# Optimization experiments

Hardware: AMD Instinct MI355X
Metric: run time of the kernel (lower is better)

The kernel has to match this reference:

```python
import jax, jax.numpy as jnp
import numpy as np

DIM = 1024
QK = 64
V = 64
H = 8
PD = 21
HD = QK // H  # 8
SCALE = HD ** -0.5


def _ln(x, g, b, eps=1e-5):
    mu = jnp.mean(x, axis=-1, keepdims=True)
    var = jnp.var(x, axis=-1, keepdims=True)
    return (x - mu) * jax.lax.rsqrt(var + eps) * g + b


def setup_inputs() -> dict:
    key = jax.random.key(0)
    ks = jax.random.split(key, 16)
    B, L = 2, 1024
    inp = {
        'x': jax.random.normal(ks[0], (B, L, DIM), jnp.float32),
        'pair': jax.random.normal(ks[1], (B, L, L, PD), jnp.float32),
        'mask': jnp.ones((B, L), dtype=bool),
        # attention params
        'ln_g': jnp.ones((DIM,), jnp.float32),
        'ln_b': jnp.zeros((DIM,), jnp.float32),
        'Wq': jax.random.normal(ks[2], (DIM, QK), jnp.float32) * DIM ** -0.5,
        'Wv': jax.random.normal(ks[3], (DIM, QK), jnp.float32) * DIM ** -0.5,
        'bv': jnp.zeros((QK,), jnp.float32),
        'Wg': jax.random.normal(ks[4], (DIM, V), jnp.float32) * DIM ** -0.5,
        'bg': jnp.zeros((V,), jnp.float32),
        'Wo': jax.random.normal(ks[5], (V, V), jnp.float32) * V ** -0.5,
        'bo': jnp.zeros((V,), jnp.float32),
        # pair bias params
        'pln_g': jnp.ones((PD,), jnp.float32),
        'pln_b': jnp.zeros((PD,), jnp.float32),
        'Wpb': jax.random.normal(ks[6], (PD, H), jnp.float32) * PD ** -0.5,
        # OuterProductMean params
        'oln_g': jnp.ones((V,), jnp.float32),
        'oln_b': jnp.zeros((V,), jnp.float32),
        'Wr': jax.random.normal(ks[7], (V, 16), jnp.float32) * V ** -0.5,
        'br': jnp.zeros((16,), jnp.float32),
        'Wout': jax.random.normal(ks[8], (256, PD), jnp.float32) * 256 ** -0.5,
        'bout': jnp.zeros((PD,), jnp.float32),
    }
    return inp


def reference(x, pair, mask, ln_g, ln_b, Wq, Wv, bv, Wg, bg, Wo, bo,
              pln_g, pln_b, Wpb, oln_g, oln_b, Wr, br, Wout, bout):
    B, L, _ = x.shape
    nx = _ln(x, ln_g, ln_b)
    # NB: original code computes k with to_q as well (k = self.to_q(normed_x))
    q = (nx @ Wq).reshape(B, L, H, HD).transpose(0, 2, 1, 3)  # b h l d
    k = (nx @ Wq).reshape(B, L, H, HD).transpose(0, 2, 1, 3)
    v = (nx @ Wv + bv).reshape(B, L, H, HD).transpose(0, 2, 1, 3)
    gate = jax.nn.sigmoid(nx @ Wg + bg)  # b l v
    sim = jnp.einsum('bhid,bhjd->bhij', q, k) * SCALE
    bias = _ln(pair, pln_g, pln_b) @ Wpb  # b i j h
    sim = sim + jnp.transpose(bias, (0, 3, 1, 2))
    sim = jnp.where(mask[:, None, None, :], sim, -jnp.inf)
    attn = jax.nn.softmax(sim, axis=-1)
    out = jnp.einsum('bhij,bhjd->bhid', attn, v)
    out = out.transpose(0, 2, 1, 3).reshape(B, L, QK)  # b l (h d)
    out = (out * gate) @ Wo + bo  # b l v
    # OuterProductMean: out_pair[b,m,n,p] = sum_ij r[b,m,i] r[b,n,j] W3[i,j,p] + bout
    r = _ln(out, oln_g, oln_b) @ Wr + br  # b l 16
    W3 = Wout.reshape(16, 16, PD)  # flatten order (i j)
    t = jnp.einsum('bmi,ijp->bmjp', r, W3)  # b l 16 p (small)
    pair_out = jnp.einsum('bmjp,bnj->bmnp', t, r) + bout  # b m n p
    return out, pair_out
```

## Files before the change

kernel.cpp:

```cpp
#include <hip/hip_runtime.h>
#include <hip/hip_bf16.h>
#include <stdint.h>
#include <stddef.h>

typedef unsigned short u16;
typedef unsigned int   u32;

#define SCALE 0.35355339059327373f

using bfrag  = __attribute__((ext_vector_type(8))) short;
using f32x4v = __attribute__((ext_vector_type(4))) float;

__device__ __forceinline__ float bfh(u16 u) {
    union { u32 i; float f; } v; v.i = ((u32)u) << 16; return v.f;
}
__device__ __forceinline__ u16 f2bf(float f) {
    u32 x = __float_as_uint(f);
    u32 r = x + 0x7FFFu + ((x >> 16) & 1u);
    return (u16)(r >> 16);
}
__device__ __forceinline__ float dot4f(float4 a, float4 b) {
    return fmaf(a.x, b.x, fmaf(a.y, b.y, fmaf(a.z, b.z, a.w * b.w)));
}
__device__ __forceinline__ f32x4v mfma16(uint4 a, uint4 b, f32x4v c) {
    return __builtin_amdgcn_mfma_f32_16x16x32_bf16(
        __builtin_bit_cast(bfrag, a), __builtin_bit_cast(bfrag, b), c, 0, 0, 0);
}

__global__ void k_prep(const float* __restrict__ Wq, const float* __restrict__ Wv,
                       const float* __restrict__ Wg, u16* __restrict__ Wf)
{
    int tid  = blockIdx.x * 256 + threadIdx.x;
    int l    = tid & 63;
    int ctks = tid >> 6;
    int ct   = ctks % 12;
    int n    = ct * 16 + (l & 15);
    int kbase = ((ctks / 12) << 5) + ((l >> 4) << 3);
    const float* src = (n < 64) ? (Wq + n)
                     : ((n < 128) ? (Wv + n - 64) : (Wg + n - 128));
    u32 hp[4], lp[4];
    #pragma unroll
    for (int jp = 0; jp < 4; jp++) {
        float w0 = src[(size_t)(kbase + 2*jp    ) << 6];
        float w1 = src[(size_t)(kbase + 2*jp + 1) << 6];
        u16 h0 = f2bf(w0), h1 = f2bf(w1);
        u16 l0 = f2bf(w0 - bfh(h0)), l1 = f2bf(w1 - bfh(h1));
        hp[jp] = (u32)h0 | ((u32)h1 << 16);
        lp[jp] = (u32)l0 | ((u32)l1 << 16);
    }
    size_t o = (size_t)ctks * 1024 + l * 8;
    *(uint4*)(Wf + o)       = make_uint4(hp[0], hp[1], hp[2], hp[3]);
    *(uint4*)(Wf + o + 512) = make_uint4(lp[0], lp[1], lp[2], lp[3]);
}

__global__ __launch_bounds__(384) void k_lnproj(
    const float* __restrict__ x,
    const float* __restrict__ lng, const float* __restrict__ lnb,
    const u16* __restrict__ Wf,
    const float* __restrict__ bv, const float* __restrict__ bg,
    u16* __restrict__ q_ws, u16* __restrict__ v_ws, float* __restrict__ gate_ws,
    u16* __restrict__ qt_ws)
{
    __shared__ u16 sA[32768];
    const int t = threadIdx.x;
    const int w = t >> 6, lane = t & 63;
    const int rg = blockIdx.x >> 1;
    const int cc = blockIdx.x & 1;

    float4 gv[4], bb[4];
    #pragma unroll
    for (int s = 0; s < 4; s++) {
        gv[s] = ((const float4*)lng)[s * 64 + lane];
        bb[s] = ((const float4*)lnb)[s * 64 + lane];
    }
    const int kb_base = lane >> 1;
    const int jo = (lane & 1) << 2;
    for (int row = w; row < 16; row += 6) {
        int gr  = (rg << 4) + row;
        const float4* xrow = (const float4*)(x + (size_t)gr * 1024);
        float4 xv[4]; float sum = 0.f, sq = 0.f;
        #pragma unroll
        for (int s = 0; s < 4; s++) {
            float4 d = xrow[s * 64 + lane];
            xv[s] = d;
            sum += (d.x + d.y) + (d.z + d.w);
            sq = fmaf(d.x, d.x, sq); sq = fmaf(d.y, d.y, sq);
            sq = fmaf(d.z, d.z, sq); sq = fmaf(d.w, d.w, sq);
        }
        #pragma unroll
        for (int m = 1; m < 64; m <<= 1) {
            sum += __shfl_xor(sum, m, 64);
            sq  += __shfl_xor(sq,  m, 64);
        }
        float mu  = sum * (1.f / 1024.f);
        float var = sq * (1.f / 1024.f) - mu * mu;
        float rs  = rsqrtf(var + 1e-5f);
        #pragma unroll
        for (int s = 0; s < 4; s++) {
            float n0 = (xv[s].x - mu) * rs * gv[s].x + bb[s].x;
            float n1 = (xv[s].y - mu) * rs * gv[s].y + bb[s].y;
            float n2 = (xv[s].z - mu) * rs * gv[s].z + bb[s].z;
            float n3 = (xv[s].w - mu) * rs * gv[s].w + bb[s].w;
            u16 h0 = f2bf(n0), h1 = f2bf(n1), h2 = f2bf(n2), h3 = f2bf(n3);
            u16 l0 = f2bf(n0 - bfh(h0)), l1 = f2bf(n1 - bfh(h1));
            u16 l2 = f2bf(n2 - bfh(h2)), l3 = f2bf(n3 - bfh(h3));
            int kb  = (s << 5) + kb_base;
            int idx = ((kb << 4) + (row ^ (kb & 7))) * 8 + jo;
            uint2 hw, lw;
            hw.x = (u32)h0 | ((u32)h1 << 16); hw.y = (u32)h2 | ((u32)h3 << 16);
            lw.x = (u32)l0 | ((u32)l1 << 16); lw.y = (u32)l2 | ((u32)l3 << 16);
            *(uint2*)&sA[idx]         = hw;
            *(uint2*)&sA[16384 + idx] = lw;
        }
    }
    __syncthreads();

    const int cin  = lane & 15;
    const int kgrp = lane >> 4;
    const int ct   = cc * 6 + w;
    const uint4* a4 = (const uint4*)sA;
    const uint4* bp = (const uint4*)Wf + (size_t)ct * 128 + lane;

    uint4 ah = a4[kgrp * 16 + (cin ^ (kgrp & 7))];
    uint4 al = a4[2048 + kgrp * 16 + (cin ^ (kgrp & 7))];
    uint4 bh = bp[0], bl = bp[64];
    f32x4v acc = {0.f, 0.f, 0.f, 0.f};

    for (int ks = 0; ks < 32; ks++) {
        int kn = ((ks + 1) & 31) * 4 + kgrp;
        int rn = cin ^ (kn & 7);
        uint4 nah = a4[kn * 16 + rn];
        uint4 nal = a4[2048 + kn * 16 + rn];
        const uint4* np = bp + ((ks < 31) ? 1536 : 0);
        uint4 nbh = np[0], nbl = np[64];

        acc = mfma16(ah, bh, acc);
        acc = mfma16(ah, bl, acc);
        acc = mfma16(al, bh, acc);

        ah = nah; al = nal; bh = nbh; bl = nbl; bp = np;
    }

    {
        int n   = (ct << 4) + cin;
        int seg = ct >> 2;
        #pragma unroll
        for (int rg4 = 0; rg4 < 4; rg4++) {
            size_t gr = (size_t)(rg << 4) + (kgrp << 2) + rg4;
            float val = acc[rg4];
            if (seg == 0) {
                q_ws[gr * 64 + n] = f2bf(val);
            } else if (seg == 1) {
                v_ws[gr * 64 + (n - 64)] = f2bf(val + bv[n - 64]);
            } else {
                float z = val + bg[n - 128];
                gate_ws[gr * 64 + (n - 128)] = 1.f / (1.f + __expf(-z));
            }
        }
    }

    if (cc == 0) {
        __syncthreads();
        if (w < 4) {
            #pragma unroll
            for (int rg4 = 0; rg4 < 4; rg4++)
                sA[(((ct << 4) + cin) << 4) + (kgrp << 2) + rg4] = f2bf(acc[rg4]);
        }
        __syncthreads();
        if (t < 128) {
            int f = t >> 1, rh = t & 1;
            uint4 val = *(const uint4*)(sA + (f << 4) + (rh << 3));
            size_t off = ((size_t)(rg >> 6) << 16) + ((size_t)f << 10)
                       + ((size_t)(rg & 63) << 4) + (rh << 3);
            *(uint4*)(qt_ws + off) = val;
        }
    }
}

__global__ __launch_bounds__(256, 4) void k_attn(
    const float* __restrict__ pairp,
    const u16* __restrict__ q_ws, const u16* __restrict__ qt_ws,
    const u16* __restrict__ v_ws,
    const float* __restrict__ gate_ws,
    const float* __restrict__ plng, const float* __restrict__ plnb,
    const float* __restrict__ Wpb,
    const float* __restrict__ Wo, const float* __restrict__ bo,
    const float* __restrict__ olng, const float* __restrict__ olnb,
    const float* __restrict__ Wr, const float* __restrict__ br,
    float* __restrict__ out0, float* __restrict__ r_ws)
{
    const int SP = 1032;
    __shared__ __align__(16) float s_sim[8 * 1032];
    __shared__ __align__(16) float s_pool[1344];
    __shared__ float s_q[64];
    __shared__ float s_GW2[168];
    __shared__ float s_SG[8];
    __shared__ float s_C[8];
    __shared__ float s_inv[8];

    const int t = threadIdx.x;
    const int w = t >> 6, lane = t & 63;
    const int b = blockIdx.x >> 10;

    if (t < 168) {
        int p = t >> 3, r = t & 7, w2 = r >> 1, k = r & 1;
        s_GW2[((p << 2) + w2) * 2 + k] = plng[p] * Wpb[p*8 + w2 + (k << 2)];
    }
    if (t < 8) {
        float sg = 0.f, cc = 0.f;
        for (int p = 0; p < 21; p++) {
            float wv = Wpb[p*8 + t];
            sg = fmaf(plng[p], wv, sg);
            cc = fmaf(plnb[p], wv, cc);
        }
        s_SG[t] = sg; s_C[t] = cc;
    }
    if (t < 64) s_q[t] = bfh(q_ws[(size_t)blockIdx.x * 64 + t]);
    __syncthreads();

    const int h0 = w, h1 = w + 4;
    float qi0[8], qi1[8];
    #pragma unroll
    for (int d = 0; d < 8; d++) {
        qi0[d] = s_q[(h0 << 3) + d];
        qi1[d] = s_q[(h1 << 3) + d];
    }
    const float SG0 = s_SG[h0], SG1 = s_SG[h1];
    const float C0  = s_C[h0],  C1  = s_C[h1];
    const u16* qtb = qt_ws + ((size_t)b << 16);
    const float2* gw2 = (const float2*)s_GW2;

    float mx0 = -1e30f, mx1 = -1e30f;

    const float4* src4 = (const float4*)(pairp + (size_t)blockIdx.x * 21504);
    float4 pA0, pA1, pB0, pB1;
    pA0 = src4[t];
    pA1 = (t < 80) ? src4[256 + t] : pA0;
    pB0 = src4[336 + t];
    pB1 = (t < 80) ? src4[336 + 256 + t] : pB0;

    auto chunk_compute = [&](int u) {
        int jj = (u << 6) + lane;
        const u16* q0p = qtb + ((size_t)h0 << 13) + jj;
        const u16* q1p = qtb + ((size_t)h1 << 13) + jj;
        float qa0[8], qa1[8];
        #pragma unroll
        for (int d = 0; d < 8; d++) {
            qa0[d] = bfh(q0p[(size_t)d << 10]);
            qa1[d] = bfh(q1p[(size_t)d << 10]);
        }
        const float* xr = s_pool + lane * 21;
        float s = 0.f, q2 = 0.f, a0 = 0.f, a1 = 0.f;
        #pragma unroll
        for (int p = 0; p < 21; p++) {
            float vx = xr[p];
            float2 g = gw2[(p << 2) + w];
            s += vx; q2 = fmaf(vx, vx, q2);
            a0 = fmaf(vx, g.x, a0);
            a1 = fmaf(vx, g.y, a1);
        }
        float m   = s * (1.f / 21.f);
        float var = q2 * (1.f / 21.f) - m * m;
        float rsb = rsqrtf(var + 1e-5f);
        float qk0 = qa0[0] * qi0[0], qk1 = qa1[0] * qi1[0];
        #pragma unroll
        for (int d = 1; d < 8; d++) {
            qk0 = fmaf(qa0[d], qi0[d], qk0);
            qk1 = fmaf(qa1[d], qi1[d], qk1);
        }
        float sim0 = fmaf(qk0, SCALE, fmaf(rsb, a0 - m * SG0, C0));
        float sim1 = fmaf(qk1, SCALE, fmaf(rsb, a1 - m * SG1, C1));
        s_sim[h0 * SP + jj] = sim0;
        s_sim[h1 * SP + jj] = sim1;
        mx0 = fmaxf(mx0, sim0);
        mx1 = fmaxf(mx1, sim1);
    };

    for (int u = 0; u < 16; u += 2) {
        ((float4*)s_pool)[t] = pA0;
        if (t < 80) ((float4*)s_pool)[256 + t] = pA1;
        __syncthreads();
        if (u + 2 < 16) {
            pA0 = src4[(u + 2) * 336 + t];
            if (t < 80) pA1 = src4[(u + 2) * 336 + 256 + t];
        }
        chunk_compute(u);
        __syncthreads();
        ((float4*)s_pool)[t] = pB0;
        if (t < 80) ((float4*)s_pool)[256 + t] = pB1;
        __syncthreads();
        if (u + 3 < 16) {
            pB0 = src4[(u + 3) * 336 + t];
            if (t < 80) pB1 = src4[(u + 3) * 336 + 256 + t];
        }
        chunk_compute(u + 1);
        __syncthreads();
    }

    #pragma unroll
    for (int msk = 1; msk < 64; msk <<= 1) {
        mx0 = fmaxf(mx0, __shfl_xor(mx0, msk, 64));
        mx1 = fmaxf(mx1, __shfl_xor(mx1, msk, 64));
    }
    float4* r0 = (float4*)(s_sim + h0 * SP);
    float4* r1 = (float4*)(s_sim + h1 * SP);
    float ss0 = 0.f, ss1 = 0.f;
    #pragma unroll
    for (int u = 0; u < 4; u++) {
        int i4 = lane + (u << 6);
        float4 v0 = r0[i4], v1 = r1[i4];
        v0.x = __expf(v0.x - mx0); v0.y = __expf(v0.y - mx0);
        v0.z = __expf(v0.z - mx0); v0.w = __expf(v0.w - mx0);
        v1.x = __expf(v1.x - mx1); v1.y = __expf(v1.y - mx1);
        v1.z = __expf(v1.z - mx1); v1.w = __expf(v1.w - mx1);
        r0[i4] = v0; r1[i4] = v1;
        ss0 += (v0.x + v0.y) + (v0.z + v0.w);
        ss1 += (v1.x + v1.y) + (v1.z + v1.w);
    }
    #pragma unroll
    for (int msk = 1; msk < 64; msk <<= 1) {
        ss0 += __shfl_xor(ss0, msk, 64);
        ss1 += __shfl_xor(ss1, msk, 64);
    }
    if (lane == 0) {
        s_inv[h0] = 1.f / ss0;
        s_inv[h1] = 1.f / ss1;
    }
    __syncthreads();

    float* s_po = s_pool;
    float* s_go = s_pool + 256;
    float* s_no = s_pool + 320;
    {
        int o = t & 63, ch = t >> 6, h = o >> 3;
        const float4* srow = (const float4*)(s_sim + h * SP + (ch << 8));
        const u16* vp = v_ws + ((size_t)b << 16) + ((size_t)(ch << 8) << 6) + o;
        float a0 = 0.f, a1 = 0.f, a2 = 0.f, a3 = 0.f;
        for (int j4 = 0; j4 < 64; j4++) {
            float4 sv = srow[j4];
            size_t jb = (size_t)(j4 << 2) << 6;
            a0 = fmaf(sv.x, bfh(vp[jb]),       a0);
            a1 = fmaf(sv.y, bfh(vp[jb + 64]),  a1);
            a2 = fmaf(sv.z, bfh(vp[jb + 128]), a2);
            a3 = fmaf(sv.w, bfh(vp[jb + 192]), a3);
        }
        s_po[t] = (a0 + a1) + (a2 + a3);
    }
    __syncthreads();
    if (t < 64) {
        int h = t >> 3;
        float a = (s_po[t] + s_po[64 + t] + s_po[128 + t] + s_po[192 + t]) * s_inv[h];
        float g = gate_ws[(size_t)blockIdx.x * 64 + t];
        s_go[t] = a * g;
    }
    __syncthreads();
    if (t < 64) {
        float acc = bo[t];
        #pragma unroll 8
        for (int o2 = 0; o2 < 64; o2++)
            acc = fmaf(s_go[o2], Wo[(o2 << 6) + t], acc);
        out0[(size_t)blockIdx.x * 64 + t] = acc;
        float s1 = acc, s2 = acc * acc;
        #pragma unroll
        for (int msk = 1; msk < 64; msk <<= 1) {
            s1 += __shfl_xor(s1, msk, 64);
            s2 += __shfl_xor(s2, msk, 64);
        }
        float mu = s1 * (1.f / 64.f);
        float var = s2 * (1.f / 64.f) - mu * mu;
        float rs = rsqrtf(var + 1e-5f);
        s_no[t] = (acc - mu) * rs * olng[t] + olnb[t];
    }
    __syncthreads();
    if (t < 16) {
        float acc = br[t];
        #pragma unroll 8
        for (int o2 = 0; o2 < 64; o2++)
            acc = fmaf(s_no[o2], Wr[(o2 << 4) + t], acc);
        r_ws[(size_t)blockIdx.x * 16 + t] = acc;
    }
}

__global__ __launch_bounds__(256, 4) void k_outer(
    const float* __restrict__ r_ws,
    const float* __restrict__ Wout, const float* __restrict__ bout,
    float* __restrict__ outp)
{
    __shared__ float s_rm[16];
    __shared__ float s_tt[21 * 16];
    __shared__ float s_b[21];
    const int t = threadIdx.x;
    const int b = blockIdx.x >> 10;

    if (t < 16) s_rm[t] = r_ws[(size_t)blockIdx.x * 16 + t];
    if (t >= 32 && t < 53) s_b[t - 32] = bout[t - 32];
    __syncthreads();
    for (int idx = t; idx < 336; idx += 256) {
        int j = idx & 15, p = idx >> 4;
        float acc = 0.f;
        #pragma unroll
        for (int i = 0; i < 16; i++)
            acc = fmaf(s_rm[i], Wout[(size_t)((i << 4) + j) * 21 + p], acc);
        s_tt[p * 16 + j] = acc;
    }
    __syncthreads();
    if (t < 252) {
        int p = t % 21, g = t / 21;
        const float4* tt = (const float4*)(s_tt + p * 16);
        float4 t0 = tt[0], t1 = tt[1], t2 = tt[2], t3 = tt[3];
        float bb = s_b[p];
        const float4* rb = (const float4*)(r_ws + ((size_t)b << 14));
        float* ob = outp + (size_t)blockIdx.x * 21504 + p;
        #pragma unroll 2
        for (int n = g; n < 1024; n += 12) {
            const float4* rp = rb + (n << 2);
            float d0 = dot4f(t0, rp[0]);
            float d1 = dot4f(t1, rp[1]);
            float d2 = dot4f(t2, rp[2]);
            float d3 = dot4f(t3, rp[3]);
            ob[n * 21] = bb + ((d0 + d1) + (d2 + d3));
        }
    }
}

extern "C" void kernel_launch(void* const* d_in, const int* in_sizes, int n_in,
                              void* d_out, int out_size, void* d_ws, size_t ws_size,
                              hipStream_t stream)
{
    const float* x    = (const float*)d_in[0];
    const float* pr   = (const float*)d_in[1];
    const float* lng  = (const float*)d_in[3];
    const float* lnb  = (const float*)d_in[4];
    const float* Wq   = (const float*)d_in[5];
    const float* Wv   = (const float*)d_in[6];
    const float* bv   = (const float*)d_in[7];
    const float* Wg   = (const float*)d_in[8];
    const float* bg   = (const float*)d_in[9];
    const float* Wo   = (const float*)d_in[10];
    const float* bo   = (const float*)d_in[11];
    const float* plng = (const float*)d_in[12];
    const float* plnb = (const float*)d_in[13];
    const float* Wpb  = (const float*)d_in[14];
    const float* olng = (const float*)d_in[15];
    const float* olnb = (const float*)d_in[16];
    const float* Wr   = (const float*)d_in[17];
    const float* br   = (const float*)d_in[18];
    const float* Wout = (const float*)d_in[19];
    const float* bout = (const float*)d_in[20];

    const size_t BIG = 2097152, RSZ = 131072;
    char* scratch;
    float* r_ws = (float*)d_ws;
    if (ws_size >= BIG + RSZ) {
        scratch = (char*)d_ws + RSZ;
    } else {
        scratch = (char*)d_out + (size_t)out_size * 4 - BIG;
    }
    u16*   Wf      = (u16*)  (scratch);
    u16*   q_ws    = (u16*)  (scratch + 786432);
    u16*   v_ws    = (u16*)  (scratch + 1048576);
    float* gate_ws = (float*)(scratch + 1310720);
    u16*   qt_ws   = (u16*)  (scratch + 1835008);
    float* out = (float*)d_out;

    k_prep  <<<96,   256, 0, stream>>>(Wq, Wv, Wg, Wf);
    k_lnproj<<<256,  384, 0, stream>>>(x, lng, lnb, Wf, bv, bg,
                                       q_ws, v_ws, gate_ws, qt_ws);
    k_attn  <<<2048, 256, 0, stream>>>(pr, q_ws, qt_ws, v_ws, gate_ws,
                                       plng, plnb, Wpb,
                                       Wo, bo, olng, olnb, Wr, br, out, r_ws);
    k_outer <<<2048, 256, 0, stream>>>(r_ws, Wout, bout, out + 131072);
}
```

Measured before the change: 485.6 us.

## Keep attention scores in registers and use transposed V layout

The projection kernel now also writes V in a transposed per-head layout, the same way it already does for Q. The attention kernel keeps each lane's 16 scores per head in registers instead of a large shared-memory sim buffer. It computes P·V with per-lane partial sums reduced by wave shuffles, and double-buffers the pair-tile staging in shared memory. The aim is to cut shared-memory footprint and traffic and raise occupancy, at the cost of more registers and many shuffle reductions, since the launch-bounds occupancy hint was removed.

```diff
diff --git a/kernel.cpp b/kernel.cpp
--- a/kernel.cpp
+++ b/kernel.cpp
@@ -58,8 +58,8 @@
     const float* __restrict__ lng, const float* __restrict__ lnb,
     const u16* __restrict__ Wf,
     const float* __restrict__ bv, const float* __restrict__ bg,
-    u16* __restrict__ q_ws, u16* __restrict__ v_ws, float* __restrict__ gate_ws,
-    u16* __restrict__ qt_ws)
+    u16* __restrict__ q_ws, float* __restrict__ gate_ws,
+    u16* __restrict__ qt_ws, u16* __restrict__ vt_ws)
 {
     __shared__ u16 sA[32768];
     const int t = threadIdx.x;
@@ -141,6 +141,7 @@
         ah = nah; al = nal; bh = nbh; bl = nbl; bp = np;
     }
 
+    u16 vb16[4];
     {
         int n   = (ct << 4) + cin;
         int seg = ct >> 2;
@@ -151,7 +152,7 @@
             if (seg == 0) {
                 q_ws[gr * 64 + n] = f2bf(val);
             } else if (seg == 1) {
-                v_ws[gr * 64 + (n - 64)] = f2bf(val + bv[n - 64]);
+                vb16[rg4] = f2bf(val + bv[n - 64]);
             } else {
                 float z = val + bg[n - 128];
                 gate_ws[gr * 64 + (n - 128)] = 1.f / (1.f + __expf(-z));
@@ -159,28 +160,42 @@
         }
     }
 
-    if (cc == 0) {
-        __syncthreads();
-        if (w < 4) {
-            #pragma unroll
-            for (int rg4 = 0; rg4 < 4; rg4++)
-                sA[(((ct << 4) + cin) << 4) + (kgrp << 2) + rg4] = f2bf(acc[rg4]);
-        }
-        __syncthreads();
-        if (t < 128) {
+    __syncthreads();
+    if (cc == 0 && w < 4) {
+        #pragma unroll
+        for (int rg4 = 0; rg4 < 4; rg4++)
+            sA[(((ct << 4) + cin) << 4) + (kgrp << 2) + rg4] = f2bf(acc[rg4]);
+    }
+    if ((ct >> 2) == 1) {
+        int vl = (((ct << 4) + cin) - 64) & 31;
+        #pragma unroll
+        for (int rg4 = 0; rg4 < 4; rg4++)
+            sA[1024 + (vl << 4) + (kgrp << 2) + rg4] = vb16[rg4];
+    }
+    __syncthreads();
+    {
+        int bidx = rg >> 6, rl = rg & 63;
+        if (cc == 0 && t < 128) {
             int f = t >> 1, rh = t & 1;
             uint4 val = *(const uint4*)(sA + (f << 4) + (rh << 3));
-            size_t off = ((size_t)(rg >> 6) << 16) + ((size_t)f << 10)
-                       + ((size_t)(rg & 63) << 4) + (rh << 3);
-            *(uint4*)(qt_ws + off) = val;
-        }
-    }
-}
-
-__global__ __launch_bounds__(256, 4) void k_attn(
+            *(uint4*)(qt_ws + ((size_t)bidx << 16) + ((size_t)f << 10)
+                            + (rl << 4) + (rh << 3)) = val;
+        }
+        if (t >= 128 && t < 192) {
+            int t2 = t - 128;
+            int fl = t2 >> 1, rh = t2 & 1;
+            uint4 val = *(const uint4*)(sA + 1024 + (fl << 4) + (rh << 3));
+            int f = fl + (cc << 5);
+            *(uint4*)(vt_ws + ((size_t)bidx << 16) + ((size_t)f << 10)
+                            + (rl << 4) + (rh << 3)) = val;
+        }
+    }
+}
+
+__global__ __launch_bounds__(256) void k_attn(
     const float* __restrict__ pairp,
     const u16* __restrict__ q_ws, const u16* __restrict__ qt_ws,
-    const u16* __restrict__ v_ws,
+    const u16* __restrict__ vt_ws,
     const float* __restrict__ gate_ws,
     const float* __restrict__ plng, const float* __restrict__ plnb,
     const float* __restrict__ Wpb,
@@ -189,14 +204,14 @@
     const float* __restrict__ Wr, const float* __restrict__ br,
     float* __restrict__ out0, float* __restrict__ r_ws)
 {
-    const int SP = 1032;
-    __shared__ __align__(16) float s_sim[8 * 1032];
-    __shared__ __align__(16) float s_pool[1344];
+    __shared__ __align__(16) float s_pair[2][1344];
     __shared__ float s_q[64];
     __shared__ float s_GW2[168];
     __shared__ float s_SG[8];
     __shared__ float s_C[8];
-    __shared__ float s_inv[8];
+    __shared__ float s_ov[64];
+    __shared__ float s_go[64];
+    __shared__ float s_no[64];
 
     const int t = threadIdx.x;
     const int w = t >> 6, lane = t & 63;
@@ -216,6 +231,15 @@
         s_SG[t] = sg; s_C[t] = cc;
     }
     if (t < 64) s_q[t] = bfh(q_ws[(size_t)blockIdx.x * 64 + t]);
+
+    const float4* src4 = (const float4*)(pairp + (size_t)blockIdx.x * 21504);
+    float4 rA = src4[t], rB;
+    if (t < 80) rB = src4[256 + t];
+    ((float4*)s_pair[0])[t] = rA;
+    if (t < 80) ((float4*)s_pair[0])[256 + t] = rB;
+    rA = src4[336 + t];
+    if (t < 80) rB = src4[336 + 256 + t];
+
     __syncthreads();
 
     const int h0 = w, h1 = w + 4;
@@ -227,29 +251,32 @@
     }
     const float SG0 = s_SG[h0], SG1 = s_SG[h1];
     const float C0  = s_C[h0],  C1  = s_C[h1];
-    const u16* qtb = qt_ws + ((size_t)b << 16);
+    const u16* q0p = qt_ws + ((size_t)b << 16) + ((size_t)h0 << 13) + lane;
+    const u16* q1p = qt_ws + ((size_t)b << 16) + ((size_t)h1 << 13) + lane;
     const float2* gw2 = (const float2*)s_GW2;
 
+    float p0[16], p1[16];
     float mx0 = -1e30f, mx1 = -1e30f;
 
-    const float4* src4 = (const float4*)(pairp + (size_t)blockIdx.x * 21504);
-    float4 pA0, pA1, pB0, pB1;
-    pA0 = src4[t];
-    pA1 = (t < 80) ? src4[256 + t] : pA0;
-    pB0 = src4[336 + t];
-    pB1 = (t < 80) ? src4[336 + 256 + t] : pB0;
-
-    auto chunk_compute = [&](int u) {
-        int jj = (u << 6) + lane;
-        const u16* q0p = qtb + ((size_t)h0 << 13) + jj;
-        const u16* q1p = qtb + ((size_t)h1 << 13) + jj;
+    #pragma unroll
+    for (int u = 0; u < 16; u++) {
+        if (u) __syncthreads();
+        if (u < 15) {
+            float4* nb = (float4*)s_pair[(u + 1) & 1];
+            nb[t] = rA;
+            if (t < 80) nb[256 + t] = rB;
+            if (u < 14) {
+                rA = src4[(u + 2) * 336 + t];
+                if (t < 80) rB = src4[(u + 2) * 336 + 256 + t];
+            }
+        }
         float qa0[8], qa1[8];
         #pragma unroll
         for (int d = 0; d < 8; d++) {
-            qa0[d] = bfh(q0p[(size_t)d << 10]);
-            qa1[d] = bfh(q1p[(size_t)d << 10]);
-        }
-        const float* xr = s_pool + lane * 21;
+            qa0[d] = bfh(q0p[(d << 10) + (u << 6)]);
+            qa1[d] = bfh(q1p[(d << 10) + (u << 6)]);
+        }
+        const float* xr = s_pair[u & 1] + lane * 21;
         float s = 0.f, q2 = 0.f, a0 = 0.f, a1 = 0.f;
         #pragma unroll
         for (int p = 0; p < 21; p++) {
@@ -270,31 +297,8 @@
         }
         float sim0 = fmaf(qk0, SCALE, fmaf(rsb, a0 - m * SG0, C0));
         float sim1 = fmaf(qk1, SCALE, fmaf(rsb, a1 - m * SG1, C1));
-        s_sim[h0 * SP + jj] = sim0;
-        s_sim[h1 * SP + jj] = sim1;
-        mx0 = fmaxf(mx0, sim0);
-        mx1 = fmaxf(mx1, sim1);
-    };
-
-    for (int u = 0; u < 16; u += 2) {
-        ((float4*)s_pool)[t] = pA0;
-        if (t < 80) ((float4*)s_pool)[256 + t] = pA1;
-        __syncthreads();
-        if (u + 2 < 16) {
-            pA0 = src4[(u + 2) * 336 + t];
-            if (t < 80) pA1 = src4[(u + 2) * 336 + 256 + t];
-        }
-        chunk_compute(u);
-        __syncthreads();
-        ((float4*)s_pool)[t] = pB0;
-        if (t < 80) ((float4*)s_pool)[256 + t] = pB1;
-        __syncthreads();
-        if (u + 3 < 16) {
-            pB0 = src4[(u + 3) * 336 + t];
-            if (t < 80) pB1 = src4[(u + 3) * 336 + 256 + t];
-        }
-        chunk_compute(u + 1);
-        __syncthreads();
+        p0[u] = sim0; p1[u] = sim1;
+        mx0 = fmaxf(mx0, sim0); mx1 = fmaxf(mx1, sim1);
     }
 
     #pragma unroll
@@ -302,56 +306,50 @@
         mx0 = fmaxf(mx0, __shfl_xor(mx0, msk, 64));
         mx1 = fmaxf(mx1, __shfl_xor(mx1, msk, 64));
     }
-    float4* r0 = (float4*)(s_sim + h0 * SP);
-    float4* r1 = (float4*)(s_sim + h1 * SP);
     float ss0 = 0.f, ss1 = 0.f;
     #pragma unroll
-    for (int u = 0; u < 4; u++) {
-        int i4 = lane + (u << 6);
-        float4 v0 = r0[i4], v1 = r1[i4];
-        v0.x = __expf(v0.x - mx0); v0.y = __expf(v0.y - mx0);
-        v0.z = __expf(v0.z - mx0); v0.w = __expf(v0.w - mx0);
-        v1.x = __expf(v1.x - mx1); v1.y = __expf(v1.y - mx1);
-        v1.z = __expf(v1.z - mx1); v1.w = __expf(v1.w - mx1);
-        r0[i4] = v0; r1[i4] = v1;
-        ss0 += (v0.x + v0.y) + (v0.z + v0.w);
-        ss1 += (v1.x + v1.y) + (v1.z + v1.w);
+    for (int u = 0; u < 16; u++) {
+        p0[u] = __expf(p0[u] - mx0); ss0 += p0[u];
+        p1[u] = __expf(p1[u] - mx1); ss1 += p1[u];
     }
     #pragma unroll
     for (int msk = 1; msk < 64; msk <<= 1) {
         ss0 += __shfl_xor(ss0, msk, 64);
         ss1 += __shfl_xor(ss1, msk, 64);
     }
+    float inv0 = 1.f / ss0, inv1 = 1.f / ss1;
+
+    const u16* vt0 = vt_ws + ((size_t)b << 16) + ((size_t)h0 << 13) + lane;
+    const u16* vt1 = vt_ws + ((size_t)b << 16) + ((size_t)h1 << 13) + lane;
+    float o0[8] = {0,0,0,0,0,0,0,0}, o1[8] = {0,0,0,0,0,0,0,0};
+    #pragma unroll
+    for (int u = 0; u < 16; u++) {
+        #pragma unroll
+        for (int d = 0; d < 8; d++) {
+            o0[d] = fmaf(p0[u], bfh(vt0[(d << 10) + (u << 6)]), o0[d]);
+            o1[d] = fmaf(p1[u], bfh(vt1[(d << 10) + (u << 6)]), o1[d]);
+        }
+    }
+    #pragma unroll
+    for (int msk = 1; msk < 64; msk <<= 1) {
+        #pragma unroll
+        for (int d = 0; d < 8; d++) {
+            o0[d] += __shfl_xor(o0[d], msk, 64);
+            o1[d] += __shfl_xor(o1[d], msk, 64);
+        }
+    }
     if (lane == 0) {
-        s_inv[h0] = 1.f / ss0;
-        s_inv[h1] = 1.f / ss1;
-    }
-    __syncthreads();
-
-    float* s_po = s_pool;
-    float* s_go = s_pool + 256;
-    float* s_no = s_pool + 320;
-    {
-        int o = t & 63, ch = t >> 6, h = o >> 3;
-        const float4* srow = (const float4*)(s_sim + h * SP + (ch << 8));
-        const u16* vp = v_ws + ((size_t)b << 16) + ((size_t)(ch << 8) << 6) + o;
-        float a0 = 0.f, a1 = 0.f, a2 = 0.f, a3 = 0.f;
-        for (int j4 = 0; j4 < 64; j4++) {
-            float4 sv = srow[j4];
-            size_t jb = (size_t)(j4 << 2) << 6;
-            a0 = fmaf(sv.x, bfh(vp[jb]),       a0);
-            a1 = fmaf(sv.y, bfh(vp[jb + 64]),  a1);
-            a2 = fmaf(sv.z, bfh(vp[jb + 128]), a2);
-            a3 = fmaf(sv.w, bfh(vp[jb + 192]), a3);
-        }
-        s_po[t] = (a0 + a1) + (a2 + a3);
-    }
-    __syncthreads();
+        #pragma unroll
+        for (int d = 0; d < 8; d++) {
+            s_ov[(h0 << 3) + d] = o0[d] * inv0;
+            s_ov[(h1 << 3) + d] = o1[d] * inv1;
+        }
+    }
+    __syncthreads();
+
     if (t < 64) {
-        int h = t >> 3;
-        float a = (s_po[t] + s_po[64 + t] + s_po[128 + t] + s_po[192 + t]) * s_inv[h];
         float g = gate_ws[(size_t)blockIdx.x * 64 + t];
-        s_go[t] = a * g;
+        s_go[t] = s_ov[t] * g;
     }
     __syncthreads();
     if (t < 64) {
@@ -458,15 +456,15 @@
     }
     u16*   Wf      = (u16*)  (scratch);
     u16*   q_ws    = (u16*)  (scratch + 786432);
-    u16*   v_ws    = (u16*)  (scratch + 1048576);
-    float* gate_ws = (float*)(scratch + 1310720);
-    u16*   qt_ws   = (u16*)  (scratch + 1835008);
+    float* gate_ws = (float*)(scratch + 1048576);
+    u16*   qt_ws   = (u16*)  (scratch + 1572864);
+    u16*   vt_ws   = (u16*)  (scratch + 1835008);
     float* out = (float*)d_out;
 
     k_prep  <<<96,   256, 0, stream>>>(Wq, Wv, Wg, Wf);
     k_lnproj<<<256,  384, 0, stream>>>(x, lng, lnb, Wf, bv, bg,
-                                       q_ws, v_ws, gate_ws, qt_ws);
-    k_attn  <<<2048, 256, 0, stream>>>(pr, q_ws, qt_ws, v_ws, gate_ws,
+                                       q_ws, gate_ws, qt_ws, vt_ws);
+    k_attn  <<<2048, 256, 0, stream>>>(pr, q_ws, qt_ws, vt_ws, gate_ws,
                                        plng, plnb, Wpb,
                                        Wo, bo, olng, olnb, Wr, br, out, r_ws);
     k_outer <<<2048, 256, 0, stream>>>(r_ws, Wout, bout, out + 131072);
```

Result: slower. 515.3 us (+6.1%).
